# Kernel tuning notes

Measured on AMD Instinct MI355X. Metric: run time of the kernel, lower is better.

## Reference

```python
import jax, jax.numpy as jnp
import numpy as np
from itertools import combinations

Nt, Nrf, Nk, FEAT, BATCH = 64, 4, 8, 512, 1024
Ng = Nt // Nk                      # 8
_MAX = len(list(combinations(range(Ng), Nrf)))  # 70
CSETSIZE = int(2 ** np.floor(np.log2(_MAX)))    # 64
SQRT_NRF = np.float32(np.sqrt(Nrf))


def _generate_antenna_selection_set(num_target):
    """Max-hamming-distance antenna selection set (numpy, matches torch code)."""
    combs = list(combinations(range(Ng), Nrf))
    maxSize = len(combs)
    globalSet = np.zeros((maxSize, Nt, Nrf), np.float32)
    for i, act in enumerate(combs):
        for j, a in enumerate(act):
            globalSet[i, a * Nk:a * Nk + Nk, j] = 1.0
    gsum = globalSet.sum(-1)  # (maxSize, Nt)
    selectSet = np.zeros((num_target, Nt, Nrf), np.float32)
    available = []
    for idx in range(num_target):
        if len(available) == 0:
            available = list(range(maxSize))
        if idx == 0:
            hd = np.zeros(len(available))
        else:
            sel = selectSet[:idx].sum(-1)            # (idx, Nt)
            cand = gsum[np.array(available)]          # (nAvail, Nt)
            hd = (sel[None, :, :] != cand[:, None, :]).sum(axis=(1, 2))
        sid = available[int(np.argmax(hd))]
        selectSet[idx] = globalSet[sid]
        available.remove(sid)
    return selectSet


def setup_inputs() -> dict:
    key = jax.random.key(0)
    ks = jax.random.split(key, 7)
    s = 1.0 / np.sqrt(FEAT)
    DDIM = CSETSIZE * Nrf * Nrf
    return {
        "x": jax.random.normal(ks[0], (BATCH, FEAT), jnp.float32),
        "W_A": jax.random.normal(ks[1], (Nt, FEAT), jnp.float32) * s,
        "b_A": jax.random.normal(ks[2], (Nt,), jnp.float32) * s,
        "W_Dr": jax.random.normal(ks[3], (DDIM, FEAT), jnp.float32) * s,
        "b_Dr": jax.random.normal(ks[4], (DDIM,), jnp.float32) * s,
        "W_Di": jax.random.normal(ks[5], (DDIM, FEAT), jnp.float32) * s,
        "b_Di": jax.random.normal(ks[6], (DDIM,), jnp.float32) * s,
        "CSet": jnp.asarray(_generate_antenna_selection_set(CSETSIZE)),
    }


def reference(x, W_A, b_A, W_Dr, b_Dr, W_Di, b_Di, CSet):
    B = x.shape[0]
    theta = x @ W_A.T + b_A                          # (B, Nt)
    cosT, sinT = jnp.cos(theta), jnp.sin(theta)
    eye = jnp.eye(Nt, dtype=x.dtype)
    A_real = (cosT[:, :, None] * eye)[:, None]       # (B, 1, Nt, Nt) diag-embed
    A_imag = (sinT[:, :, None] * eye)[:, None]
    D_real = (x @ W_Dr.T + b_Dr).reshape(B, CSETSIZE, Nrf, Nrf)
    D_imag = (x @ W_Di.T + b_Di).reshape(B, CSETSIZE, Nrf, Nrf)
    # diag(cos) @ C == row-scale of C (identical math to the dense matmul)
    ArC = cosT[:, None, :, None] * CSet[None]        # (B, CSetSize, Nt, Nrf)
    AiC = sinT[:, None, :, None] * CSet[None]
    ArCDr = ArC @ D_real
    ArCDi = ArC @ D_imag
    AiCDr = AiC @ D_real
    AiCDi = AiC @ D_imag
    V_real = ArCDr - AiCDi                           # (B, CSetSize, Nt, Nrf)
    V_imag = ArCDi + AiCDr
    V_F = jnp.sqrt(jnp.sum(V_real ** 2 + V_imag ** 2, axis=(2, 3)))
    V_F = V_F[:, :, None, None]
    D_real_n = SQRT_NRF * D_real / V_F
    D_imag_n = SQRT_NRF * D_imag / V_F
    return (A_real, A_imag, D_real_n, D_imag_n, CSet)
```

## Files before the change

kernel.cpp:

```cpp
#include <hip/hip_runtime.h>
#include <math.h>

#define BATCH 1024
#define FEAT  512
#define NT    64
#define DDIM  1024

typedef __attribute__((ext_vector_type(8))) short  short8;
typedef __attribute__((ext_vector_type(4))) float  floatx4;

#define AIMG_OFF  0
#define BIMG_OFF  1048576

__device__ __forceinline__ unsigned short bf16rne(float f) {
    unsigned int u = __float_as_uint(f);
    return (unsigned short)((u + 0x7fffu + ((u >> 16) & 1u)) >> 16);
}

__device__ __forceinline__ void gld16(const unsigned char* g, unsigned char* l) {
    __builtin_amdgcn_global_load_lds(
        (const __attribute__((address_space(1))) unsigned int*)g,
        (__attribute__((address_space(3))) unsigned int*)l, 16, 0, 0);
}

__global__ __launch_bounds__(256) void k0_convert(
    const float* __restrict__ x,
    const float* __restrict__ W_Dr,
    const float* __restrict__ W_Di,
    unsigned char* __restrict__ ws)
{
    unsigned short* aimg = (unsigned short*)(ws + AIMG_OFF);
    unsigned short* bimg = (unsigned short*)(ws + BIMG_OFF);
    const int gtid = blockIdx.x * 256 + threadIdx.x;
    #pragma unroll
    for (int v = 0; v < 3; ++v) {
        const int idx = gtid + v * 65536;
        const float* src;
        unsigned short* dst;
        if (idx < 65536) {
            const int rt = idx >> 12, kb = (idx >> 9) & 7;
            const int r  = (idx >> 3) & 63, c = idx & 7;
            src = x + ((size_t)(rt * 64 + r) * FEAT + kb * 64 + c * 8);
            dst = aimg + ((rt * 8 + kb) * 4096 + r * 64 + ((c ^ (r & 7)) * 8));
        } else {
            const int j  = idx - 65536;
            const int ct = j >> 12, kb = (j >> 9) & 7;
            const int n  = (j >> 3) & 63, c = j & 7;
            const int g = n >> 5, h = (n >> 4) & 1, pos = n & 15;
            const float* wrow =
                (h ? W_Di : W_Dr) + (size_t)(ct * 32 + g * 16 + pos) * FEAT;
            src = wrow + kb * 64 + c * 8;
            dst = bimg + ((ct * 8 + kb) * 4096 + n * 64 + ((c ^ (n & 7)) * 8));
        }
        const float4 v0 = *(const float4*)src;
        const float4 v1 = *(const float4*)(src + 4);
        short8 o;
        o[0] = (short)bf16rne(v0.x); o[1] = (short)bf16rne(v0.y);
        o[2] = (short)bf16rne(v0.z); o[3] = (short)bf16rne(v0.w);
        o[4] = (short)bf16rne(v1.x); o[5] = (short)bf16rne(v1.y);
        o[6] = (short)bf16rne(v1.z); o[7] = (short)bf16rne(v1.w);
        *(short8*)dst = o;
    }
}

__global__ __launch_bounds__(256) void k1_mega(
    const unsigned char* __restrict__ ws,
    const float* __restrict__ x,
    const float* __restrict__ W_A,
    const float* __restrict__ b_A,
    const float* __restrict__ b_Dr,
    const float* __restrict__ b_Di,
    const float* __restrict__ cset,
    float* __restrict__ out)
{
    __shared__ __align__(16) unsigned char smem[32768];

    const int beta = blockIdx.x;
    const int tid  = threadIdx.x;

    if (beta < 512) {
        const int rt   = beta & 15;
        const int ct   = beta >> 4;
        const int lane = tid & 63;
        const int wv   = tid >> 6;
        const int ln   = lane & 15;
        const int quad = lane >> 4;
        const int row0 = rt * 64;

        const unsigned char* Atiles = ws + AIMG_OFF + (size_t)rt * 8 * 8192;
        const unsigned char* Btiles = ws + BIMG_OFF + (size_t)ct * 8 * 8192;

        const int g0 = (wv * 2 + 0) * 1024;
        const int g1 = (wv * 2 + 1) * 1024;
        const int lo = lane * 16;

        floatx4 acc[4] = {{0,0,0,0},{0,0,0,0},{0,0,0,0},{0,0,0,0}};

        {
            unsigned char* La = smem;
            unsigned char* Lb = smem + 8192;
            gld16(Atiles + g0 + lo, La + g0);
            gld16(Atiles + g1 + lo, La + g1);
            gld16(Btiles + g0 + lo, Lb + g0);
            gld16(Btiles + g1 + lo, Lb + g1);
        }

        const int rowOffA = (wv * 16 + ln) * 128;
        const int swz = ln & 7;
        int cur = 0;

        #pragma unroll 1
        for (int kb = 0; kb < 8; ++kb) {
            __syncthreads();
            if (kb < 7) {
                const unsigned char* At = Atiles + (kb + 1) * 8192;
                const unsigned char* Bt = Btiles + (kb + 1) * 8192;
                unsigned char* La = smem + (cur ^ 1) * 16384;
                unsigned char* Lb = La + 8192;
                gld16(At + g0 + lo, La + g0);
                gld16(At + g1 + lo, La + g1);
                gld16(Bt + g0 + lo, Lb + g0);
                gld16(Bt + g1 + lo, Lb + g1);
            }
            const unsigned char* La = smem + cur * 16384;
            const unsigned char* Lb = La + 8192;
            #pragma unroll
            for (int ks = 0; ks < 2; ++ks) {
                const int ca = ((ks * 4 + quad) ^ swz) * 16;
                const short8 a = *(const short8*)(La + rowOffA + ca);
                #pragma unroll
                for (int t = 0; t < 4; ++t) {
                    const short8 b = *(const short8*)(Lb + (t * 16 + ln) * 128 + ca);
                    acc[t] = __builtin_amdgcn_mfma_f32_16x16x32_bf16(a, b, acc[t], 0, 0, 0);
                }
            }
            cur ^= 1;
        }

        const size_t drn = (size_t)2 * BATCH * 4096;
        const size_t din = drn + (size_t)BATCH * DDIM;
        const int woff = ct * 32;
        #pragma unroll
        for (int p = 0; p < 2; ++p) {
            const int colg = woff + p * 16 + ln;
            const float br = b_Dr[colg];
            const float bi = b_Di[colg];
            float dr[4], di[4], ps[4];
            #pragma unroll
            for (int i = 0; i < 4; ++i) {
                dr[i] = acc[2 * p][i] + br;
                di[i] = acc[2 * p + 1][i] + bi;
                ps[i] = dr[i] * dr[i] + di[i] * di[i];
            }
            #pragma unroll
            for (int i = 0; i < 4; ++i) {
                ps[i] += __shfl_xor(ps[i], 1);
                ps[i] += __shfl_xor(ps[i], 2);
                ps[i] += __shfl_xor(ps[i], 4);
                ps[i] += __shfl_xor(ps[i], 8);
            }
            #pragma unroll
            for (int i = 0; i < 4; ++i) {
                const float scale = 2.0f / sqrtf(8.0f * ps[i]);
                const size_t row_g = (size_t)(row0 + wv * 16 + quad * 4 + i);
                out[drn + row_g * DDIM + colg] = dr[i] * scale;
                out[din + row_g * DDIM + colg] = di[i] * scale;
            }
        }
    } else if (beta < 4608) {
        const int fb = beta - 512;
        const int b  = fb >> 2;
        const int rg = fb & 3;
        const int tl = tid >> 4;
        const int j  = tid & 15;
        const int t  = rg * 16 + tl;

        const float* xr = x   + (size_t)b * FEAT + j * 4;
        const float* wr = W_A + (size_t)t * FEAT + j * 4;
        float4 a = {0.f, 0.f, 0.f, 0.f};
        #pragma unroll
        for (int it = 0; it < 8; ++it) {
            const float4 xv = *(const float4*)(xr + it * 64);
            const float4 wv = *(const float4*)(wr + it * 64);
            a.x = fmaf(xv.x, wv.x, a.x);
            a.y = fmaf(xv.y, wv.y, a.y);
            a.z = fmaf(xv.z, wv.z, a.z);
            a.w = fmaf(xv.w, wv.w, a.w);
        }
        float th = (a.x + a.y) + (a.z + a.w);
        th += __shfl_xor(th, 1);
        th += __shfl_xor(th, 2);
        th += __shfl_xor(th, 4);
        th += __shfl_xor(th, 8);
        th += b_A[t];

        float4 vr = {0.f, 0.f, 0.f, 0.f};
        float4 vi = {0.f, 0.f, 0.f, 0.f};
        if ((t >> 2) == j) {
            float s, c;
            sincosf(th, &s, &c);
            ((float*)&vr)[t & 3] = c;
            ((float*)&vi)[t & 3] = s;
        }
        const size_t off = (size_t)b * 4096 + t * 64 + j * 4;
        *(float4*)(out + off) = vr;
        *(float4*)(out + (size_t)BATCH * 4096 + off) = vi;
    } else {
        const int cb = beta - 4608;
        const size_t base = (size_t)2 * BATCH * 4096 + (size_t)2 * BATCH * DDIM;
        ((float4*)(out + base))[cb * 256 + tid] = ((const float4*)cset)[cb * 256 + tid];
    }
}

extern "C" void kernel_launch(void* const* d_in, const int* in_sizes, int n_in,
                              void* d_out, int out_size, void* d_ws, size_t ws_size,
                              hipStream_t stream) {
    const float* x    = (const float*)d_in[0];
    const float* W_A  = (const float*)d_in[1];
    const float* b_A  = (const float*)d_in[2];
    const float* W_Dr = (const float*)d_in[3];
    const float* b_Dr = (const float*)d_in[4];
    const float* W_Di = (const float*)d_in[5];
    const float* b_Di = (const float*)d_in[6];
    const float* CSet = (const float*)d_in[7];
    float* out = (float*)d_out;
    unsigned char* ws = (unsigned char*)d_ws;

    k0_convert<<<256, 256, 0, stream>>>(x, W_Dr, W_Di, ws);
    k1_mega<<<4624, 256, 0, stream>>>(ws, x, W_A, b_A, b_Dr, b_Di, CSet, out);
}
```

Baseline: 107.2 us.

## Fuse bf16 conversion into GEMM tile loads, dropping the separate convert kernel

Removes the standalone fp32-to-bf16 conversion kernel and its workspace round-trip. The GEMM blocks now load fp32 x and W rows straight into registers, convert them to bf16, and write swizzled tiles to LDS, prefetching the next k-block into registers during compute. This saves one kernel launch and the extra global write and read of the bf16 images. In exchange, every column tile repeats the conversion, and the async global-to-LDS loads become register-staged loads with more VGPR pressure.

Result: slower. 110.2 us (+2.8%).

```diff
diff --git a/kernel.cpp b/kernel.cpp
--- a/kernel.cpp
+++ b/kernel.cpp
@@ -9,66 +9,27 @@
 typedef __attribute__((ext_vector_type(8))) short  short8;
 typedef __attribute__((ext_vector_type(4))) float  floatx4;
 
-#define AIMG_OFF  0
-#define BIMG_OFF  1048576
-
 __device__ __forceinline__ unsigned short bf16rne(float f) {
     unsigned int u = __float_as_uint(f);
     return (unsigned short)((u + 0x7fffu + ((u >> 16) & 1u)) >> 16);
 }
 
-__device__ __forceinline__ void gld16(const unsigned char* g, unsigned char* l) {
-    __builtin_amdgcn_global_load_lds(
-        (const __attribute__((address_space(1))) unsigned int*)g,
-        (__attribute__((address_space(3))) unsigned int*)l, 16, 0, 0);
+__device__ __forceinline__ short8 cvt8(float4 a, float4 b) {
+    short8 o;
+    o[0] = (short)bf16rne(a.x); o[1] = (short)bf16rne(a.y);
+    o[2] = (short)bf16rne(a.z); o[3] = (short)bf16rne(a.w);
+    o[4] = (short)bf16rne(b.x); o[5] = (short)bf16rne(b.y);
+    o[6] = (short)bf16rne(b.z); o[7] = (short)bf16rne(b.w);
+    return o;
 }
 
-__global__ __launch_bounds__(256) void k0_convert(
-    const float* __restrict__ x,
-    const float* __restrict__ W_Dr,
-    const float* __restrict__ W_Di,
-    unsigned char* __restrict__ ws)
-{
-    unsigned short* aimg = (unsigned short*)(ws + AIMG_OFF);
-    unsigned short* bimg = (unsigned short*)(ws + BIMG_OFF);
-    const int gtid = blockIdx.x * 256 + threadIdx.x;
-    #pragma unroll
-    for (int v = 0; v < 3; ++v) {
-        const int idx = gtid + v * 65536;
-        const float* src;
-        unsigned short* dst;
-        if (idx < 65536) {
-            const int rt = idx >> 12, kb = (idx >> 9) & 7;
-            const int r  = (idx >> 3) & 63, c = idx & 7;
-            src = x + ((size_t)(rt * 64 + r) * FEAT + kb * 64 + c * 8);
-            dst = aimg + ((rt * 8 + kb) * 4096 + r * 64 + ((c ^ (r & 7)) * 8));
-        } else {
-            const int j  = idx - 65536;
-            const int ct = j >> 12, kb = (j >> 9) & 7;
-            const int n  = (j >> 3) & 63, c = j & 7;
-            const int g = n >> 5, h = (n >> 4) & 1, pos = n & 15;
-            const float* wrow =
-                (h ? W_Di : W_Dr) + (size_t)(ct * 32 + g * 16 + pos) * FEAT;
-            src = wrow + kb * 64 + c * 8;
-            dst = bimg + ((ct * 8 + kb) * 4096 + n * 64 + ((c ^ (n & 7)) * 8));
-        }
-        const float4 v0 = *(const float4*)src;
-        const float4 v1 = *(const float4*)(src + 4);
-        short8 o;
-        o[0] = (short)bf16rne(v0.x); o[1] = (short)bf16rne(v0.y);
-        o[2] = (short)bf16rne(v0.z); o[3] = (short)bf16rne(v0.w);
-        o[4] = (short)bf16rne(v1.x); o[5] = (short)bf16rne(v1.y);
-        o[6] = (short)bf16rne(v1.z); o[7] = (short)bf16rne(v1.w);
-        *(short8*)dst = o;
-    }
-}
-
-__global__ __launch_bounds__(256) void k1_mega(
-    const unsigned char* __restrict__ ws,
+__global__ __launch_bounds__(256) void k_mega(
     const float* __restrict__ x,
     const float* __restrict__ W_A,
     const float* __restrict__ b_A,
+    const float* __restrict__ W_Dr,
     const float* __restrict__ b_Dr,
+    const float* __restrict__ W_Di,
     const float* __restrict__ b_Di,
     const float* __restrict__ cset,
     float* __restrict__ out)
@@ -87,43 +48,51 @@
         const int quad = lane >> 4;
         const int row0 = rt * 64;
 
-        const unsigned char* Atiles = ws + AIMG_OFF + (size_t)rt * 8 * 8192;
-        const unsigned char* Btiles = ws + BIMG_OFF + (size_t)ct * 8 * 8192;
+        const int r  = tid >> 2;
+        const int cp = (tid & 3) * 2;
+        const int s  = r & 7;
+        const int d0 = r * 128 + ((cp ^ s) * 16);
+        const int d1 = r * 128 + (((cp + 1) ^ s) * 16);
+        const float* srcA = x + (size_t)(row0 + r) * FEAT + cp * 8;
+        const int g = r >> 5, h = (r >> 4) & 1, pos = r & 15;
+        const float* srcB =
+            (h ? W_Di : W_Dr) + (size_t)(ct * 32 + g * 16 + pos) * FEAT + cp * 8;
 
-        const int g0 = (wv * 2 + 0) * 1024;
-        const int g1 = (wv * 2 + 1) * 1024;
-        const int lo = lane * 16;
+        float4 ra0 = *(const float4*)(srcA + 0);
+        float4 ra1 = *(const float4*)(srcA + 4);
+        float4 ra2 = *(const float4*)(srcA + 8);
+        float4 ra3 = *(const float4*)(srcA + 12);
+        float4 rb0 = *(const float4*)(srcB + 0);
+        float4 rb1 = *(const float4*)(srcB + 4);
+        float4 rb2 = *(const float4*)(srcB + 8);
+        float4 rb3 = *(const float4*)(srcB + 12);
 
         floatx4 acc[4] = {{0,0,0,0},{0,0,0,0},{0,0,0,0},{0,0,0,0}};
-
-        {
-            unsigned char* La = smem;
-            unsigned char* Lb = smem + 8192;
-            gld16(Atiles + g0 + lo, La + g0);
-            gld16(Atiles + g1 + lo, La + g1);
-            gld16(Btiles + g0 + lo, Lb + g0);
-            gld16(Btiles + g1 + lo, Lb + g1);
-        }
-
         const int rowOffA = (wv * 16 + ln) * 128;
         const int swz = ln & 7;
         int cur = 0;
 
         #pragma unroll 1
         for (int kb = 0; kb < 8; ++kb) {
+            unsigned char* La = smem + cur * 16384;
+            unsigned char* Lb = La + 8192;
+            *(short8*)(La + d0) = cvt8(ra0, ra1);
+            *(short8*)(La + d1) = cvt8(ra2, ra3);
+            *(short8*)(Lb + d0) = cvt8(rb0, rb1);
+            *(short8*)(Lb + d1) = cvt8(rb2, rb3);
             __syncthreads();
             if (kb < 7) {
-                const unsigned char* At = Atiles + (kb + 1) * 8192;
-                const unsigned char* Bt = Btiles + (kb + 1) * 8192;
-                unsigned char* La = smem + (cur ^ 1) * 16384;
-                unsigned char* Lb = La + 8192;
-                gld16(At + g0 + lo, La + g0);
-                gld16(At + g1 + lo, La + g1);
-                gld16(Bt + g0 + lo, Lb + g0);
-                gld16(Bt + g1 + lo, Lb + g1);
+                const float* pA = srcA + (kb + 1) * 64;
+                const float* pB = srcB + (kb + 1) * 64;
+                ra0 = *(const float4*)(pA + 0);
+                ra1 = *(const float4*)(pA + 4);
+                ra2 = *(const float4*)(pA + 8);
+                ra3 = *(const float4*)(pA + 12);
+                rb0 = *(const float4*)(pB + 0);
+                rb1 = *(const float4*)(pB + 4);
+                rb2 = *(const float4*)(pB + 8);
+                rb3 = *(const float4*)(pB + 12);
             }
-            const unsigned char* La = smem + cur * 16384;
-            const unsigned char* Lb = La + 8192;
             #pragma unroll
             for (int ks = 0; ks < 2; ++ks) {
                 const int ca = ((ks * 4 + quad) ^ swz) * 16;
@@ -197,10 +166,10 @@
         float4 vr = {0.f, 0.f, 0.f, 0.f};
         float4 vi = {0.f, 0.f, 0.f, 0.f};
         if ((t >> 2) == j) {
-            float s, c;
-            sincosf(th, &s, &c);
-            ((float*)&vr)[t & 3] = c;
-            ((float*)&vi)[t & 3] = s;
+            float sn, cs;
+            sincosf(th, &sn, &cs);
+            ((float*)&vr)[t & 3] = cs;
+            ((float*)&vi)[t & 3] = sn;
         }
         const size_t off = (size_t)b * 4096 + t * 64 + j * 4;
         *(float4*)(out + off) = vr;
@@ -224,8 +193,6 @@
     const float* b_Di = (const float*)d_in[6];
     const float* CSet = (const float*)d_in[7];
     float* out = (float*)d_out;
-    unsigned char* ws = (unsigned char*)d_ws;
 
-    k0_convert<<<256, 256, 0, stream>>>(x, W_Dr, W_Di, ws);
-    k1_mega<<<4624, 256, 0, stream>>>(ws, x, W_A, b_A, b_Dr, b_Di, CSet, out);
+    k_mega<<<4624, 256, 0, stream>>>(x, W_A, b_A, W_Dr, b_Dr, W_Di, b_Di, CSet, out);
 }
```

## Precompute theta in prep kernel and use nontemporal stores for outputs

Applied to the files above, without the earlier changes.

Moves the x·W_A^T theta projection out of the A-fill blocks and into extra blocks of the prep kernel, which write it to workspace. Before, each of the 4096 fill blocks redid a 512-length dot product per row. The fill blocks now only read one theta, run sincos and write the diagonal-embedded output. All large output writes switch to nontemporal stores so the streaming 32MB output does not pollute the cache. The cost is an extra workspace round-trip and a larger prep launch.

After: 103.4 us. 3.5% less time.

```diff
diff --git a/kernel.cpp b/kernel.cpp
--- a/kernel.cpp
+++ b/kernel.cpp
@@ -11,6 +11,7 @@
 
 #define AIMG_OFF  0
 #define BIMG_OFF  1048576
+#define THETA_OFF 3145728
 
 __device__ __forceinline__ unsigned short bf16rne(float f) {
     unsigned int u = __float_as_uint(f);
@@ -23,51 +24,93 @@
         (__attribute__((address_space(3))) unsigned int*)l, 16, 0, 0);
 }
 
-__global__ __launch_bounds__(256) void k0_convert(
+__device__ __forceinline__ void nt_store4(float* p, float a, float b, float c, float d) {
+    floatx4 v = {a, b, c, d};
+    __builtin_nontemporal_store(v, (floatx4*)p);
+}
+
+__device__ __forceinline__ void nt_store1(float* p, float v) {
+    __builtin_nontemporal_store(v, p);
+}
+
+__global__ __launch_bounds__(256) void k0_prep(
     const float* __restrict__ x,
+    const float* __restrict__ W_A,
+    const float* __restrict__ b_A,
     const float* __restrict__ W_Dr,
     const float* __restrict__ W_Di,
     unsigned char* __restrict__ ws)
 {
-    unsigned short* aimg = (unsigned short*)(ws + AIMG_OFF);
-    unsigned short* bimg = (unsigned short*)(ws + BIMG_OFF);
-    const int gtid = blockIdx.x * 256 + threadIdx.x;
-    #pragma unroll
-    for (int v = 0; v < 3; ++v) {
-        const int idx = gtid + v * 65536;
-        const float* src;
-        unsigned short* dst;
-        if (idx < 65536) {
-            const int rt = idx >> 12, kb = (idx >> 9) & 7;
-            const int r  = (idx >> 3) & 63, c = idx & 7;
-            src = x + ((size_t)(rt * 64 + r) * FEAT + kb * 64 + c * 8);
-            dst = aimg + ((rt * 8 + kb) * 4096 + r * 64 + ((c ^ (r & 7)) * 8));
-        } else {
-            const int j  = idx - 65536;
-            const int ct = j >> 12, kb = (j >> 9) & 7;
-            const int n  = (j >> 3) & 63, c = j & 7;
-            const int g = n >> 5, h = (n >> 4) & 1, pos = n & 15;
-            const float* wrow =
-                (h ? W_Di : W_Dr) + (size_t)(ct * 32 + g * 16 + pos) * FEAT;
-            src = wrow + kb * 64 + c * 8;
-            dst = bimg + ((ct * 8 + kb) * 4096 + n * 64 + ((c ^ (n & 7)) * 8));
-        }
-        const float4 v0 = *(const float4*)src;
-        const float4 v1 = *(const float4*)(src + 4);
-        short8 o;
-        o[0] = (short)bf16rne(v0.x); o[1] = (short)bf16rne(v0.y);
-        o[2] = (short)bf16rne(v0.z); o[3] = (short)bf16rne(v0.w);
-        o[4] = (short)bf16rne(v1.x); o[5] = (short)bf16rne(v1.y);
-        o[6] = (short)bf16rne(v1.z); o[7] = (short)bf16rne(v1.w);
-        *(short8*)dst = o;
+    const int beta = blockIdx.x;
+    const int tid  = threadIdx.x;
+
+    if (beta < 256) {
+        unsigned short* aimg = (unsigned short*)(ws + AIMG_OFF);
+        unsigned short* bimg = (unsigned short*)(ws + BIMG_OFF);
+        const int gtid = beta * 256 + tid;
+        #pragma unroll
+        for (int v = 0; v < 3; ++v) {
+            const int idx = gtid + v * 65536;
+            const float* src;
+            unsigned short* dst;
+            if (idx < 65536) {
+                const int rt = idx >> 12, kb = (idx >> 9) & 7;
+                const int r  = (idx >> 3) & 63, c = idx & 7;
+                src = x + ((size_t)(rt * 64 + r) * FEAT + kb * 64 + c * 8);
+                dst = aimg + ((rt * 8 + kb) * 4096 + r * 64 + ((c ^ (r & 7)) * 8));
+            } else {
+                const int j  = idx - 65536;
+                const int ct = j >> 12, kb = (j >> 9) & 7;
+                const int n  = (j >> 3) & 63, c = j & 7;
+                const int g = n >> 5, h = (n >> 4) & 1, pos = n & 15;
+                const float* wrow =
+                    (h ? W_Di : W_Dr) + (size_t)(ct * 32 + g * 16 + pos) * FEAT;
+                src = wrow + kb * 64 + c * 8;
+                dst = bimg + ((ct * 8 + kb) * 4096 + n * 64 + ((c ^ (n & 7)) * 8));
+            }
+            const float4 v0 = *(const float4*)src;
+            const float4 v1 = *(const float4*)(src + 4);
+            short8 o;
+            o[0] = (short)bf16rne(v0.x); o[1] = (short)bf16rne(v0.y);
+            o[2] = (short)bf16rne(v0.z); o[3] = (short)bf16rne(v0.w);
+            o[4] = (short)bf16rne(v1.x); o[5] = (short)bf16rne(v1.y);
+            o[6] = (short)bf16rne(v1.z); o[7] = (short)bf16rne(v1.w);
+            *(short8*)dst = o;
+        }
+    } else {
+        float* theta = (float*)(ws + THETA_OFF);
+        const int tb = beta - 256;
+        const int hi = tid >> 4;
+        const int j  = tid & 15;
+        #pragma unroll 1
+        for (int p = 0; p < 16; ++p) {
+            const int d = p * 16 + hi;
+            const int b = tb * 4 + (d >> 6);
+            const int t = d & 63;
+            const float* xr = x   + (size_t)b * FEAT + j * 4;
+            const float* wr = W_A + (size_t)t * FEAT + j * 4;
+            float4 a = {0.f, 0.f, 0.f, 0.f};
+            #pragma unroll
+            for (int it = 0; it < 8; ++it) {
+                const float4 xv = *(const float4*)(xr + it * 64);
+                const float4 wv = *(const float4*)(wr + it * 64);
+                a.x = fmaf(xv.x, wv.x, a.x);
+                a.y = fmaf(xv.y, wv.y, a.y);
+                a.z = fmaf(xv.z, wv.z, a.z);
+                a.w = fmaf(xv.w, wv.w, a.w);
+            }
+            float th = (a.x + a.y) + (a.z + a.w);
+            th += __shfl_xor(th, 1);
+            th += __shfl_xor(th, 2);
+            th += __shfl_xor(th, 4);
+            th += __shfl_xor(th, 8);
+            if (j == 0) theta[tb * 256 + d] = th + b_A[t];
+        }
     }
 }
 
 __global__ __launch_bounds__(256) void k1_mega(
     const unsigned char* __restrict__ ws,
-    const float* __restrict__ x,
-    const float* __restrict__ W_A,
-    const float* __restrict__ b_A,
     const float* __restrict__ b_Dr,
     const float* __restrict__ b_Di,
     const float* __restrict__ cset,
@@ -163,11 +206,12 @@
             for (int i = 0; i < 4; ++i) {
                 const float scale = 2.0f / sqrtf(8.0f * ps[i]);
                 const size_t row_g = (size_t)(row0 + wv * 16 + quad * 4 + i);
-                out[drn + row_g * DDIM + colg] = dr[i] * scale;
-                out[din + row_g * DDIM + colg] = di[i] * scale;
+                nt_store1(&out[drn + row_g * DDIM + colg], dr[i] * scale);
+                nt_store1(&out[din + row_g * DDIM + colg], di[i] * scale);
             }
         }
     } else if (beta < 4608) {
+        const float* theta = (const float*)(ws + THETA_OFF);
         const int fb = beta - 512;
         const int b  = fb >> 2;
         const int rg = fb & 3;
@@ -175,40 +219,27 @@
         const int j  = tid & 15;
         const int t  = rg * 16 + tl;
 
-        const float* xr = x   + (size_t)b * FEAT + j * 4;
-        const float* wr = W_A + (size_t)t * FEAT + j * 4;
-        float4 a = {0.f, 0.f, 0.f, 0.f};
-        #pragma unroll
-        for (int it = 0; it < 8; ++it) {
-            const float4 xv = *(const float4*)(xr + it * 64);
-            const float4 wv = *(const float4*)(wr + it * 64);
-            a.x = fmaf(xv.x, wv.x, a.x);
-            a.y = fmaf(xv.y, wv.y, a.y);
-            a.z = fmaf(xv.z, wv.z, a.z);
-            a.w = fmaf(xv.w, wv.w, a.w);
-        }
-        float th = (a.x + a.y) + (a.z + a.w);
-        th += __shfl_xor(th, 1);
-        th += __shfl_xor(th, 2);
-        th += __shfl_xor(th, 4);
-        th += __shfl_xor(th, 8);
-        th += b_A[t];
-
-        float4 vr = {0.f, 0.f, 0.f, 0.f};
-        float4 vi = {0.f, 0.f, 0.f, 0.f};
+        const float th = theta[b * NT + t];
+
+        float r0 = 0.f, r1 = 0.f, r2 = 0.f, r3 = 0.f;
+        float i0 = 0.f, i1 = 0.f, i2 = 0.f, i3 = 0.f;
         if ((t >> 2) == j) {
-            float s, c;
-            sincosf(th, &s, &c);
-            ((float*)&vr)[t & 3] = c;
-            ((float*)&vi)[t & 3] = s;
+            float sn, cs;
+            sincosf(th, &sn, &cs);
+            const int k = t & 3;
+            if (k == 0) { r0 = cs; i0 = sn; }
+            else if (k == 1) { r1 = cs; i1 = sn; }
+            else if (k == 2) { r2 = cs; i2 = sn; }
+            else { r3 = cs; i3 = sn; }
         }
         const size_t off = (size_t)b * 4096 + t * 64 + j * 4;
-        *(float4*)(out + off) = vr;
-        *(float4*)(out + (size_t)BATCH * 4096 + off) = vi;
+        nt_store4(out + off, r0, r1, r2, r3);
+        nt_store4(out + (size_t)BATCH * 4096 + off, i0, i1, i2, i3);
     } else {
         const int cb = beta - 4608;
         const size_t base = (size_t)2 * BATCH * 4096 + (size_t)2 * BATCH * DDIM;
-        ((float4*)(out + base))[cb * 256 + tid] = ((const float4*)cset)[cb * 256 + tid];
+        const floatx4 v = ((const floatx4*)cset)[cb * 256 + tid];
+        __builtin_nontemporal_store(v, &((floatx4*)(out + base))[cb * 256 + tid]);
     }
 }
 
@@ -226,6 +257,6 @@
     float* out = (float*)d_out;
     unsigned char* ws = (unsigned char*)d_ws;
 
-    k0_convert<<<256, 256, 0, stream>>>(x, W_Dr, W_Di, ws);
-    k1_mega<<<4624, 256, 0, stream>>>(ws, x, W_A, b_A, b_Dr, b_Di, CSet, out);
-}
+    k0_prep<<<512, 256, 0, stream>>>(x, W_A, b_A, W_Dr, W_Di, ws);
+    k1_mega<<<4624, 256, 0, stream>>>(ws, b_Dr, b_Di, CSet, out);
+}
```
